# Kernel optimization log

Measured on AMD Instinct MI355X. Metric: run time of the kernel, lower is better.

## Reference

```python
import jax, jax.numpy as jnp
import numpy as np

N_GROUPS = 32
EPS = 1e-5


def group_norm(x, gamma, beta):
    b, c, h, w = x.shape
    xg = x.reshape(b, N_GROUPS, c // N_GROUPS, h, w)
    mean = xg.mean(axis=(2, 3, 4), keepdims=True)
    var = xg.var(axis=(2, 3, 4), keepdims=True)
    xn = ((xg - mean) * jax.lax.rsqrt(var + EPS)).reshape(b, c, h, w)
    return xn * gamma[None, :, None, None] + beta[None, :, None, None]


def conv1x1(x, W, b):
    # x: [b,c,h,w], W: [out,in], b: [out]
    return jnp.einsum('bchw,oc->bohw', x, W) + b[None, :, None, None]


def setup_inputs() -> dict:
    key = jax.random.key(0)
    ks = jax.random.split(key, 6)
    B, C, H, W = 8, 256, 64, 64
    s = 1.0 / np.sqrt(C)
    return {
        'x': jax.random.normal(ks[0], (B, C, H, W), dtype=jnp.float32),
        'norm_gamma': jnp.ones((C,), jnp.float32),
        'norm_beta': jnp.zeros((C,), jnp.float32),
        'Wq': jax.random.normal(ks[1], (C, C), jnp.float32) * s,
        'bq': jnp.zeros((C,), jnp.float32),
        'Wk': jax.random.normal(ks[2], (C, C), jnp.float32) * s,
        'bk': jnp.zeros((C,), jnp.float32),
        'Wv': jax.random.normal(ks[3], (C, C), jnp.float32) * s,
        'bv': jnp.zeros((C,), jnp.float32),
        'Wo': jax.random.normal(ks[4], (C, C), jnp.float32) * s,
        'bo': jnp.zeros((C,), jnp.float32),
    }


def reference(x, norm_gamma, norm_beta, Wq, bq, Wk, bk, Wv, bv, Wo, bo):
    b, c, h, w = x.shape
    hn = group_norm(x, norm_gamma, norm_beta)
    q = conv1x1(hn, Wq, bq).reshape(b, c, h * w)  # [b,c,hw]
    k = conv1x1(hn, Wk, bk).reshape(b, c, h * w)
    v = conv1x1(hn, Wv, bv).reshape(b, c, h * w)
    # scores[b,i,j] = sum_c q[b,c,i] * k[b,c,j]; scale is int(c)*-0.5
    # (faithful to the source, which multiplies by -0.5*c, NOT c**-0.5)
    scores = jnp.einsum('bci,bcj->bij', q, k) * (c * -0.5)
    attn = jax.nn.softmax(scores, axis=2)  # softmax over j (keys)
    # h_[b,c,i] = sum_j v[b,c,j] * attn[b,i,j]
    h_ = jnp.einsum('bcj,bij->bci', v, attn).reshape(b, c, h, w)
    # source applies self.out to the ORIGINAL input x and adds attention output
    return h_ + conv1x1(x, Wo, bo)
```

## Files before the change

kernel.cpp:

```cpp
#include <hip/hip_runtime.h>
#include <hip/hip_bf16.h>


typedef __attribute__((ext_vector_type(8))) short bf16x8;
typedef __attribute__((ext_vector_type(4))) short s16x4;
typedef __attribute__((ext_vector_type(8))) short s16x8;
typedef __attribute__((ext_vector_type(4))) float f32x4;

#define MFMA16(a, b, c) __builtin_amdgcn_mfma_f32_16x16x32_bf16((a), (b), (c), 0, 0, 0)

#define SCALE_Q (-184.66496523378734f)

__device__ __forceinline__ short f2bf(float f) {
  unsigned int u = __builtin_bit_cast(unsigned int, f);
  u = (u + 0x7FFFu + ((u >> 16) & 1u)) >> 16;
  return (short)(unsigned short)u;
}
__device__ __forceinline__ float bf2f(short h) {
  unsigned int u = ((unsigned int)(unsigned short)h) << 16;
  return __builtin_bit_cast(float, u);
}
__device__ __forceinline__ void async16(void* lds, const void* g) {
  __builtin_amdgcn_global_load_lds(
      (const __attribute__((address_space(1))) unsigned int*)g,
      (__attribute__((address_space(3))) unsigned int*)lds, 16, 0, 0);
}

__global__ void wsplit_k(const float* __restrict__ Wq, const float* __restrict__ Wk,
                         const float* __restrict__ Wv, const float* __restrict__ Wo,
                         short* __restrict__ whi, short* __restrict__ wlo) {
  int idx = blockIdx.x * 256 + threadIdx.x;
  int m = idx >> 16;
  int e = idx & 65535;
  const float* W = (m == 0) ? Wq : (m == 1) ? Wk : (m == 2) ? Wv : Wo;
  float v = W[e];
  short h = f2bf(v);
  whi[idx] = h;
  wlo[idx] = f2bf(v - bf2f(h));
}

__global__ void gn_stats_k(const float* __restrict__ x, float* __restrict__ stats) {
  int bg = blockIdx.x;
  int tid = threadIdx.x;
  const float* p = x + (size_t)bg * 32768;
  float s = 0.f, sq = 0.f;
  for (int it = 0; it < 32; ++it) {
    f32x4 v = *(const f32x4*)(p + (size_t)(it * 256 + tid) * 4);
    s += v[0] + v[1] + v[2] + v[3];
    sq += v[0] * v[0] + v[1] * v[1] + v[2] * v[2] + v[3] * v[3];
  }
#pragma unroll
  for (int off = 1; off < 64; off <<= 1) {
    s += __shfl_xor(s, off);
    sq += __shfl_xor(sq, off);
  }
  __shared__ float ls[4], lq[4];
  int w = tid >> 6;
  if ((tid & 63) == 0) { ls[w] = s; lq[w] = sq; }
  __syncthreads();
  if (tid == 0) {
    float S = ls[0] + ls[1] + ls[2] + ls[3];
    float Q = lq[0] + lq[1] + lq[2] + lq[3];
    float mean = S * (1.f / 32768.f);
    float var = Q * (1.f / 32768.f) - mean * mean;
    stats[bg * 2] = mean;
    stats[bg * 2 + 1] = rsqrtf(var + 1e-5f);
  }
}

__global__ void gn_apply_k(const float* __restrict__ x, const float* __restrict__ gamma,
                           const float* __restrict__ beta, const float* __restrict__ stats,
                           short* __restrict__ hn_hi, short* __restrict__ hn_lo) {
  __shared__ float tile[64 * 68];
  int tid = threadIdx.x;
  int b = blockIdx.z, c0 = blockIdx.y * 64, i0 = blockIdx.x * 64;
  int cc = tid >> 4, ich = tid & 15;
#pragma unroll
  for (int it = 0; it < 4; ++it) {
    int c = c0 + cc + it * 16;
    f32x4 vx = *(const f32x4*)(x + ((size_t)(b * 256 + c)) * 4096 + i0 + ich * 4);
    float mean = stats[(b * 32 + (c >> 3)) * 2];
    float rstd = stats[(b * 32 + (c >> 3)) * 2 + 1];
    float ga = gamma[c] * rstd;
    float be = beta[c] - mean * ga;
    f32x4 h = {vx[0] * ga + be, vx[1] * ga + be, vx[2] * ga + be, vx[3] * ga + be};
    *(f32x4*)(&tile[(cc + it * 16) * 68 + ich * 4]) = h;
  }
  __syncthreads();
  int il = tid >> 2, ch = tid & 3;
  s16x8 hv0, hv1, lv0, lv1;
#pragma unroll
  for (int u = 0; u < 16; ++u) {
    float vv = tile[(ch * 16 + u) * 68 + il];
    short h = f2bf(vv);
    short lo = f2bf(vv - bf2f(h));
    if (u < 8) { hv0[u] = h; lv0[u] = lo; } else { hv1[u - 8] = h; lv1[u - 8] = lo; }
  }
  size_t ro = ((size_t)(b * 4096 + i0 + il)) * 256 + c0 + ch * 16;
  *(s16x8*)(hn_hi + ro) = hv0;
  *(s16x8*)(hn_hi + ro + 8) = hv1;
  *(s16x8*)(hn_lo + ro) = lv0;
  *(s16x8*)(hn_lo + ro + 8) = lv1;
}

__global__ void xt_k(const float* __restrict__ x, short* __restrict__ xt) {
  __shared__ float tile[64 * 68];
  int tid = threadIdx.x;
  int b = blockIdx.z, c0 = blockIdx.y * 64, i0 = blockIdx.x * 64;
  int cc = tid >> 4, ich = tid & 15;
#pragma unroll
  for (int it = 0; it < 4; ++it) {
    int c = c0 + cc + it * 16;
    f32x4 vx = *(const f32x4*)(x + ((size_t)(b * 256 + c)) * 4096 + i0 + ich * 4);
    *(f32x4*)(&tile[(cc + it * 16) * 68 + ich * 4]) = vx;
  }
  __syncthreads();
  int il = tid >> 2, ch = tid & 3;
  s16x8 hv0, hv1;
#pragma unroll
  for (int u = 0; u < 16; ++u) {
    float vv = tile[(ch * 16 + u) * 68 + il];
    short h = f2bf(vv);
    if (u < 8) hv0[u] = h; else hv1[u - 8] = h;
  }
  size_t ro = ((size_t)(b * 4096 + i0 + il)) * 256 + c0 + ch * 16;
  *(s16x8*)(xt + ro) = hv0;
  *(s16x8*)(xt + ro + 8) = hv1;
}

__global__ __launch_bounds__(256) void proj_qk_k(
    const short* __restrict__ hn_hi, const short* __restrict__ hn_lo,
    const short* __restrict__ whi, const short* __restrict__ wlo,
    const float* __restrict__ bq, const float* __restrict__ bk,
    short* __restrict__ q_hi, short* __restrict__ q_lo,
    short* __restrict__ k_hi, short* __restrict__ k_lo) {
  int tid = threadIdx.x, w = tid >> 6, lane = tid & 63, l4 = lane & 15, g = lane >> 4;
  int iblk = blockIdx.x, y = blockIdx.y, b = blockIdx.z;
  const short* wh = whi + y * 65536;
  const short* wl = wlo + y * 65536;
  const float* bias = y ? bk : bq;
  short* ohi = (y ? k_hi : q_hi) + (size_t)b * 1048576;
  short* olo = (y ? k_lo : q_lo) + (size_t)b * 1048576;
  float scale = y ? 1.0f : SCALE_Q;
  int arow = iblk * 64 + w * 16 + l4;
  const short* ha = hn_hi + ((size_t)(b * 4096 + arow)) * 256 + g * 8;
  const short* la = hn_lo + ((size_t)(b * 4096 + arow)) * 256 + g * 8;
  f32x4 acc[16];
#pragma unroll
  for (int i = 0; i < 16; ++i) acc[i] = (f32x4){0.f, 0.f, 0.f, 0.f};
  for (int ks = 0; ks < 8; ++ks) {
    bf16x8 ah = *(const bf16x8*)(ha + ks * 32);
    bf16x8 al = *(const bf16x8*)(la + ks * 32);
#pragma unroll
    for (int ct = 0; ct < 16; ++ct) {
      bf16x8 bh = *(const bf16x8*)(wh + (ct * 16 + l4) * 256 + ks * 32 + g * 8);
      bf16x8 bl = *(const bf16x8*)(wl + (ct * 16 + l4) * 256 + ks * 32 + g * 8);
      acc[ct] = MFMA16(ah, bh, acc[ct]);
      acc[ct] = MFMA16(al, bh, acc[ct]);
      acc[ct] = MFMA16(ah, bl, acc[ct]);
    }
  }
  int orow = iblk * 64 + w * 16 + g * 4;
#pragma unroll
  for (int ct = 0; ct < 16; ++ct) {
    int c = ct * 16 + l4;
    float bsv = bias[c];
#pragma unroll
    for (int r = 0; r < 4; ++r) {
      float val = (acc[ct][r] + bsv) * scale;
      short h = f2bf(val);
      short lo = f2bf(val - bf2f(h));
      size_t off = ((size_t)(orow + r)) * 256 + c;
      ohi[off] = h;
      olo[off] = lo;
    }
  }
}

__global__ __launch_bounds__(256) void proj_v_k(
    const short* __restrict__ hn_hi, const short* __restrict__ wv_hi,
    const float* __restrict__ bv, short* __restrict__ vout) {
  int tid = threadIdx.x, w = tid >> 6, lane = tid & 63, l4 = lane & 15, g = lane >> 4;
  int jblk = blockIdx.x, cblk = blockIdx.y, b = blockIdx.z;
  int crow = cblk * 64 + w * 16 + l4;
  const short* ap = wv_hi + (size_t)crow * 256 + g * 8;
  f32x4 acc[4];
#pragma unroll
  for (int i = 0; i < 4; ++i) acc[i] = (f32x4){0.f, 0.f, 0.f, 0.f};
  for (int ks = 0; ks < 8; ++ks) {
    bf16x8 a = *(const bf16x8*)(ap + ks * 32);
#pragma unroll
    for (int jt = 0; jt < 4; ++jt) {
      bf16x8 bb = *(const bf16x8*)(hn_hi +
          ((size_t)(b * 4096 + jblk * 64 + jt * 16 + l4)) * 256 + ks * 32 + g * 8);
      acc[jt] = MFMA16(a, bb, acc[jt]);
    }
  }
#pragma unroll
  for (int jt = 0; jt < 4; ++jt) {
#pragma unroll
    for (int r = 0; r < 4; ++r) {
      int c = cblk * 64 + w * 16 + g * 4 + r;
      int j = jblk * 64 + jt * 16 + l4;
      float val = acc[jt][r] + bv[c];
      vout[((size_t)(b * 256 + c)) * 4096 + j] = f2bf(val);
    }
  }
}

__global__ __launch_bounds__(256) void outproj_k(
    const short* __restrict__ xt, const short* __restrict__ wo_hi,
    const float* __restrict__ bo, float* __restrict__ out) {
  int tid = threadIdx.x, w = tid >> 6, lane = tid & 63, l4 = lane & 15, g = lane >> 4;
  int jblk = blockIdx.x, cblk = blockIdx.y, b = blockIdx.z;
  int crow = cblk * 64 + w * 16 + l4;
  const short* ap = wo_hi + (size_t)crow * 256 + g * 8;
  f32x4 acc[4];
#pragma unroll
  for (int i = 0; i < 4; ++i) acc[i] = (f32x4){0.f, 0.f, 0.f, 0.f};
  for (int ks = 0; ks < 8; ++ks) {
    bf16x8 a = *(const bf16x8*)(ap + ks * 32);
#pragma unroll
    for (int jt = 0; jt < 4; ++jt) {
      bf16x8 bb = *(const bf16x8*)(xt +
          ((size_t)(b * 4096 + jblk * 64 + jt * 16 + l4)) * 256 + ks * 32 + g * 8);
      acc[jt] = MFMA16(a, bb, acc[jt]);
    }
  }
#pragma unroll
  for (int jt = 0; jt < 4; ++jt) {
#pragma unroll
    for (int r = 0; r < 4; ++r) {
      int c = cblk * 64 + w * 16 + g * 4 + r;
      int j = jblk * 64 + jt * 16 + l4;
      out[((size_t)(b * 256 + c)) * 4096 + j] = acc[jt][r] + bo[c];
    }
  }
}

__global__ __launch_bounds__(256, 2) void flash_k(
    const short* __restrict__ qhi, const short* __restrict__ qlo,
    const short* __restrict__ khi, const short* __restrict__ klo,
    const short* __restrict__ vv, float* __restrict__ out) {
  __shared__ short k_hi_s[8192];
  __shared__ short k_lo_s[8192];
  __shared__ short v_s[8192];
  __shared__ short p_s[2560];

  int tid = threadIdx.x, w = tid >> 6, lane = tid & 63, l4 = lane & 15, g = lane >> 4;
  int b = blockIdx.y, i0 = blockIdx.x * 64;
  size_t boff = (size_t)b * 1048576;
  const short* qh_p = qhi + boff;
  const short* ql_p = qlo + boff;
  const char* kh_g = (const char*)(khi + boff);
  const char* kl_g = (const char*)(klo + boff);
  const char* v_g = (const char*)(vv + boff);

  int qrow = i0 + w * 16 + l4;
  bf16x8 qh[8], ql[8];
#pragma unroll
  for (int ks = 0; ks < 8; ++ks) {
    qh[ks] = *(const bf16x8*)(qh_p + (size_t)qrow * 256 + ks * 32 + g * 8);
    ql[ks] = *(const bf16x8*)(ql_p + (size_t)qrow * 256 + ks * 32 + g * 8);
  }

  f32x4 oac[16];
#pragma unroll
  for (int i = 0; i < 16; ++i) oac[i] = (f32x4){0.f, 0.f, 0.f, 0.f};
  float m_cur = -1e30f, lsum = 0.f;

  int sx = (l4 & 7) << 4;
  int colx[8];
#pragma unroll
  for (int ks = 0; ks < 8; ++ks) colx[ks] = (ks * 64 + g * 16) ^ sx;
  int krow_b = l4 * 512;
  int vx = l4 * 64 + ((g ^ (l4 & 3)) << 4);
  int pwb = w * 1280 + l4 * 80 + g * 8;
  int prb = w * 1280 + l4 * 80 + g * 16;

  int ksrc[4], vsrc[4];
#pragma unroll
  for (int it = 0; it < 4; ++it) {
    int d = tid * 16 + it * 4096;
    int krow = d >> 9, kcol = d & 511;
    ksrc[it] = krow * 512 + (kcol ^ ((krow & 7) << 4));
    int vrow = d >> 6, vch = (d >> 4) & 3;
    vsrc[it] = vrow * 8192 + ((vch ^ (vrow & 3)) << 4);
  }

  char* khs = (char*)k_hi_s;
  char* kls = (char*)k_lo_s;
  char* vs = (char*)v_s;
  char* ps = (char*)p_s;

  for (int js = 0; js < 128; ++js) {
    int kgo = js * 16384;
    int vgo = js * 64;
    __syncthreads();
#pragma unroll
    for (int it = 0; it < 4; ++it) {
      int ldst = w * 1024 + it * 4096;
      async16(khs + ldst, kh_g + kgo + ksrc[it]);
      async16(kls + ldst, kl_g + kgo + ksrc[it]);
      async16(vs + ldst, v_g + vgo + vsrc[it]);
    }
    __syncthreads();

    f32x4 st0 = (f32x4){0.f, 0.f, 0.f, 0.f};
    f32x4 st1 = (f32x4){0.f, 0.f, 0.f, 0.f};
#pragma unroll
    for (int ks = 0; ks < 8; ++ks) {
      bf16x8 kh0 = *(const bf16x8*)(khs + krow_b + colx[ks]);
      bf16x8 kh1 = *(const bf16x8*)(khs + krow_b + colx[ks] + 8192);
      bf16x8 kl0 = *(const bf16x8*)(kls + krow_b + colx[ks]);
      bf16x8 kl1 = *(const bf16x8*)(kls + krow_b + colx[ks] + 8192);
      st0 = MFMA16(kh0, qh[ks], st0);
      st1 = MFMA16(kh1, qh[ks], st1);
      st0 = MFMA16(kl0, qh[ks], st0);
      st1 = MFMA16(kl1, qh[ks], st1);
      st0 = MFMA16(kh0, ql[ks], st0);
      st1 = MFMA16(kh1, ql[ks], st1);
    }

    float pmax = fmaxf(fmaxf(fmaxf(st0[0], st0[1]), fmaxf(st0[2], st0[3])),
                       fmaxf(fmaxf(st1[0], st1[1]), fmaxf(st1[2], st1[3])));
    pmax = fmaxf(pmax, __shfl_xor(pmax, 16));
    pmax = fmaxf(pmax, __shfl_xor(pmax, 32));
    if (!__all(pmax <= m_cur + 11.0f)) {
      float m_new = fmaxf(m_cur, pmax);
      float al = exp2f(m_cur - m_new);
      lsum *= al;
      int rb = g * 4;
      f32x4 av;
      av[0] = __shfl(al, rb);
      av[1] = __shfl(al, rb + 1);
      av[2] = __shfl(al, rb + 2);
      av[3] = __shfl(al, rb + 3);
#pragma unroll
      for (int ct = 0; ct < 16; ++ct) oac[ct] *= av;
      m_cur = m_new;
    }
    f32x4 e0, e1;
#pragma unroll
    for (int r = 0; r < 4; ++r) {
      e0[r] = exp2f(st0[r] - m_cur);
      e1[r] = exp2f(st1[r] - m_cur);
    }
    float lps = e0[0] + e0[1] + e0[2] + e0[3] + e1[0] + e1[1] + e1[2] + e1[3];
    lps += __shfl_xor(lps, 16);
    lps += __shfl_xor(lps, 32);
    lsum += lps;

    s16x4 pw0 = {f2bf(e0[0]), f2bf(e0[1]), f2bf(e0[2]), f2bf(e0[3])};
    s16x4 pw1 = {f2bf(e1[0]), f2bf(e1[1]), f2bf(e1[2]), f2bf(e1[3])};
    *(s16x4*)(ps + pwb) = pw0;
    *(s16x4*)(ps + pwb + 32) = pw1;
    bf16x8 pa = *(const bf16x8*)(ps + prb);
#pragma unroll
    for (int ct = 0; ct < 16; ++ct) {
      bf16x8 vb = *(const bf16x8*)(vs + vx + ct * 1024);
      oac[ct] = MFMA16(pa, vb, oac[ct]);
    }
  }

  f32x4 inv;
  {
    int rb = g * 4;
    inv[0] = 1.f / __shfl(lsum, rb);
    inv[1] = 1.f / __shfl(lsum, rb + 1);
    inv[2] = 1.f / __shfl(lsum, rb + 2);
    inv[3] = 1.f / __shfl(lsum, rb + 3);
  }
  float* ob = out + (size_t)b * 1048576;
  int irow = i0 + w * 16 + g * 4;
#pragma unroll
  for (int ct = 0; ct < 16; ++ct) {
    float* ad = ob + (size_t)(ct * 16 + l4) * 4096 + irow;
    f32x4 prev = *(const f32x4*)ad;
    f32x4 res;
#pragma unroll
    for (int r = 0; r < 4; ++r) res[r] = prev[r] + oac[ct][r] * inv[r];
    *(f32x4*)ad = res;
  }
}

extern "C" void kernel_launch(void* const* d_in, const int* in_sizes, int n_in,
                              void* d_out, int out_size, void* d_ws, size_t ws_size,
                              hipStream_t stream) {
  (void)in_sizes; (void)n_in; (void)out_size; (void)ws_size;
  const float* x = (const float*)d_in[0];
  const float* gamma = (const float*)d_in[1];
  const float* beta = (const float*)d_in[2];
  const float* Wq = (const float*)d_in[3];
  const float* bq = (const float*)d_in[4];
  const float* Wk = (const float*)d_in[5];
  const float* bk = (const float*)d_in[6];
  const float* Wv = (const float*)d_in[7];
  const float* bv = (const float*)d_in[8];
  const float* Wo = (const float*)d_in[9];
  const float* bo = (const float*)d_in[10];
  float* out = (float*)d_out;
  char* ws = (char*)d_ws;

  const size_t MB16 = 16777216;
  float* stats = (float*)(ws);
  short* whi = (short*)(ws + 4096);
  short* wlo = (short*)(ws + 4096 + 524288);
  char* base = ws + 4096 + 2 * 524288;
  short* hnhi = (short*)(base);
  short* hnlo = (short*)(base + MB16);
  short* qhi = (short*)(base + 2 * MB16);
  short* qlo = (short*)(base + 3 * MB16);
  short* khi = (short*)(base + 4 * MB16);
  short* klo = (short*)(base + 5 * MB16);
  short* vvp = (short*)(base + 6 * MB16);
  short* xt = hnhi;

  wsplit_k<<<dim3(1024), dim3(256), 0, stream>>>(Wq, Wk, Wv, Wo, whi, wlo);
  gn_stats_k<<<dim3(256), dim3(256), 0, stream>>>(x, stats);
  gn_apply_k<<<dim3(64, 4, 8), dim3(256), 0, stream>>>(x, gamma, beta, stats, hnhi, hnlo);
  proj_qk_k<<<dim3(64, 2, 8), dim3(256), 0, stream>>>(hnhi, hnlo, whi, wlo, bq, bk,
                                                      qhi, qlo, khi, klo);
  proj_v_k<<<dim3(64, 4, 8), dim3(256), 0, stream>>>(hnhi, whi + 2 * 65536, bv, vvp);
  xt_k<<<dim3(64, 4, 8), dim3(256), 0, stream>>>(x, xt);
  outproj_k<<<dim3(64, 4, 8), dim3(256), 0, stream>>>(xt, whi + 3 * 65536, bo, out);
  flash_k<<<dim3(64, 8), dim3(256), 0, stream>>>(qhi, qlo, khi, klo, vvp, out);
}
```

Before: 561.3 us.

## Fuse output projection into flash kernel and double-buffer K tiles

Removes the xt transpose and outproj kernels and computes the Wo·x projection inside the attention kernel's epilogue, adding it to the normalized attention output before a single store. The flash kernel now double-buffers K hi/lo tiles in LDS with async prefetch of the next tile, and loads V directly from global into registers. The P·V step is restructured so each wave owns a 64-channel slice for all 64 query rows, with rescale factors shared through LDS. It also raises wave priority around the score MFMAs. The exchange is an extra barrier per iteration and uncoalesced global V and x reads, which may cost more than the eliminated kernel launches and output read-modify-write.

```diff
diff --git a/kernel.cpp b/kernel.cpp
--- a/kernel.cpp
+++ b/kernel.cpp
@@ -101,31 +101,6 @@
   *(s16x8*)(hn_hi + ro + 8) = hv1;
   *(s16x8*)(hn_lo + ro) = lv0;
   *(s16x8*)(hn_lo + ro + 8) = lv1;
-}
-
-__global__ void xt_k(const float* __restrict__ x, short* __restrict__ xt) {
-  __shared__ float tile[64 * 68];
-  int tid = threadIdx.x;
-  int b = blockIdx.z, c0 = blockIdx.y * 64, i0 = blockIdx.x * 64;
-  int cc = tid >> 4, ich = tid & 15;
-#pragma unroll
-  for (int it = 0; it < 4; ++it) {
-    int c = c0 + cc + it * 16;
-    f32x4 vx = *(const f32x4*)(x + ((size_t)(b * 256 + c)) * 4096 + i0 + ich * 4);
-    *(f32x4*)(&tile[(cc + it * 16) * 68 + ich * 4]) = vx;
-  }
-  __syncthreads();
-  int il = tid >> 2, ch = tid & 3;
-  s16x8 hv0, hv1;
-#pragma unroll
-  for (int u = 0; u < 16; ++u) {
-    float vv = tile[(ch * 16 + u) * 68 + il];
-    short h = f2bf(vv);
-    if (u < 8) hv0[u] = h; else hv1[u - 8] = h;
-  }
-  size_t ro = ((size_t)(b * 4096 + i0 + il)) * 256 + c0 + ch * 16;
-  *(s16x8*)(xt + ro) = hv0;
-  *(s16x8*)(xt + ro + 8) = hv1;
 }
 
 __global__ __launch_bounds__(256) void proj_qk_k(
@@ -208,44 +183,18 @@
   }
 }
 
-__global__ __launch_bounds__(256) void outproj_k(
-    const short* __restrict__ xt, const short* __restrict__ wo_hi,
-    const float* __restrict__ bo, float* __restrict__ out) {
-  int tid = threadIdx.x, w = tid >> 6, lane = tid & 63, l4 = lane & 15, g = lane >> 4;
-  int jblk = blockIdx.x, cblk = blockIdx.y, b = blockIdx.z;
-  int crow = cblk * 64 + w * 16 + l4;
-  const short* ap = wo_hi + (size_t)crow * 256 + g * 8;
-  f32x4 acc[4];
-#pragma unroll
-  for (int i = 0; i < 4; ++i) acc[i] = (f32x4){0.f, 0.f, 0.f, 0.f};
-  for (int ks = 0; ks < 8; ++ks) {
-    bf16x8 a = *(const bf16x8*)(ap + ks * 32);
-#pragma unroll
-    for (int jt = 0; jt < 4; ++jt) {
-      bf16x8 bb = *(const bf16x8*)(xt +
-          ((size_t)(b * 4096 + jblk * 64 + jt * 16 + l4)) * 256 + ks * 32 + g * 8);
-      acc[jt] = MFMA16(a, bb, acc[jt]);
-    }
-  }
-#pragma unroll
-  for (int jt = 0; jt < 4; ++jt) {
-#pragma unroll
-    for (int r = 0; r < 4; ++r) {
-      int c = cblk * 64 + w * 16 + g * 4 + r;
-      int j = jblk * 64 + jt * 16 + l4;
-      out[((size_t)(b * 256 + c)) * 4096 + j] = acc[jt][r] + bo[c];
-    }
-  }
-}
-
-__global__ __launch_bounds__(256, 2) void flash_k(
+__global__ __launch_bounds__(256, 2) void flash3_k(
     const short* __restrict__ qhi, const short* __restrict__ qlo,
     const short* __restrict__ khi, const short* __restrict__ klo,
-    const short* __restrict__ vv, float* __restrict__ out) {
-  __shared__ short k_hi_s[8192];
-  __shared__ short k_lo_s[8192];
-  __shared__ short v_s[8192];
-  __shared__ short p_s[2560];
+    const short* __restrict__ vv, const float* __restrict__ x,
+    const short* __restrict__ wo_hi, const float* __restrict__ bo,
+    float* __restrict__ out) {
+  __shared__ short k_hi_s[2][8192];
+  __shared__ short k_lo_s[2][8192];
+  __shared__ short p_s[2048];
+  __shared__ __attribute__((aligned(16))) float albuf[64];
+  __shared__ __attribute__((aligned(16))) float flagbuf[4];
+  __shared__ __attribute__((aligned(16))) float lsmbuf[64];
 
   int tid = threadIdx.x, w = tid >> 6, lane = tid & 63, l4 = lane & 15, g = lane >> 4;
   int b = blockIdx.y, i0 = blockIdx.x * 64;
@@ -254,7 +203,7 @@
   const short* ql_p = qlo + boff;
   const char* kh_g = (const char*)(khi + boff);
   const char* kl_g = (const char*)(klo + boff);
-  const char* v_g = (const char*)(vv + boff);
+  const short* v_p = vv + boff;
 
   int qrow = i0 + w * 16 + l4;
   bf16x8 qh[8], ql[8];
@@ -264,9 +213,11 @@
     ql[ks] = *(const bf16x8*)(ql_p + (size_t)qrow * 256 + ks * 32 + g * 8);
   }
 
-  f32x4 oac[16];
-#pragma unroll
-  for (int i = 0; i < 16; ++i) oac[i] = (f32x4){0.f, 0.f, 0.f, 0.f};
+  f32x4 oac[4][4];
+#pragma unroll
+  for (int it = 0; it < 4; ++it)
+#pragma unroll
+    for (int ct = 0; ct < 4; ++ct) oac[it][ct] = (f32x4){0.f, 0.f, 0.f, 0.f};
   float m_cur = -1e30f, lsum = 0.f;
 
   int sx = (l4 & 7) << 4;
@@ -274,46 +225,55 @@
 #pragma unroll
   for (int ks = 0; ks < 8; ++ks) colx[ks] = (ks * 64 + g * 16) ^ sx;
   int krow_b = l4 * 512;
-  int vx = l4 * 64 + ((g ^ (l4 & 3)) << 4);
-  int pwb = w * 1280 + l4 * 80 + g * 8;
-  int prb = w * 1280 + l4 * 80 + g * 16;
-
-  int ksrc[4], vsrc[4];
+
+  int ksrc[4];
 #pragma unroll
   for (int it = 0; it < 4; ++it) {
     int d = tid * 16 + it * 4096;
     int krow = d >> 9, kcol = d & 511;
     ksrc[it] = krow * 512 + (kcol ^ ((krow & 7) << 4));
-    int vrow = d >> 6, vch = (d >> 4) & 3;
-    vsrc[it] = vrow * 8192 + ((vch ^ (vrow & 3)) << 4);
   }
 
   char* khs = (char*)k_hi_s;
   char* kls = (char*)k_lo_s;
-  char* vs = (char*)v_s;
   char* ps = (char*)p_s;
+  int cbase = w * 64;
+  bf16x8 vreg[4];
+
+#pragma unroll
+  for (int it = 0; it < 4; ++it) {
+    int ldst = w * 1024 + it * 4096;
+    async16(khs + ldst, kh_g + ksrc[it]);
+    async16(kls + ldst, kl_g + ksrc[it]);
+  }
 
   for (int js = 0; js < 128; ++js) {
-    int kgo = js * 16384;
-    int vgo = js * 64;
+    int cur = (js & 1) * 16384;
     __syncthreads();
-#pragma unroll
-    for (int it = 0; it < 4; ++it) {
-      int ldst = w * 1024 + it * 4096;
-      async16(khs + ldst, kh_g + kgo + ksrc[it]);
-      async16(kls + ldst, kl_g + kgo + ksrc[it]);
-      async16(vs + ldst, v_g + vgo + vsrc[it]);
-    }
-    __syncthreads();
+    if (js < 127) {
+      int kgo = (js + 1) * 16384;
+      int nxt = ((js + 1) & 1) * 16384;
+#pragma unroll
+      for (int it = 0; it < 4; ++it) {
+        int ldst = nxt + w * 1024 + it * 4096;
+        async16(khs + ldst, kh_g + kgo + ksrc[it]);
+        async16(kls + ldst, kl_g + kgo + ksrc[it]);
+      }
+    }
+#pragma unroll
+    for (int ct = 0; ct < 4; ++ct)
+      vreg[ct] = *(const bf16x8*)(v_p + (size_t)(cbase + ct * 16 + l4) * 4096 +
+                                  js * 32 + g * 8);
 
     f32x4 st0 = (f32x4){0.f, 0.f, 0.f, 0.f};
     f32x4 st1 = (f32x4){0.f, 0.f, 0.f, 0.f};
+    __builtin_amdgcn_s_setprio(1);
 #pragma unroll
     for (int ks = 0; ks < 8; ++ks) {
-      bf16x8 kh0 = *(const bf16x8*)(khs + krow_b + colx[ks]);
-      bf16x8 kh1 = *(const bf16x8*)(khs + krow_b + colx[ks] + 8192);
-      bf16x8 kl0 = *(const bf16x8*)(kls + krow_b + colx[ks]);
-      bf16x8 kl1 = *(const bf16x8*)(kls + krow_b + colx[ks] + 8192);
+      bf16x8 kh0 = *(const bf16x8*)(khs + cur + krow_b + colx[ks]);
+      bf16x8 kh1 = *(const bf16x8*)(khs + cur + krow_b + colx[ks] + 8192);
+      bf16x8 kl0 = *(const bf16x8*)(kls + cur + krow_b + colx[ks]);
+      bf16x8 kl1 = *(const bf16x8*)(kls + cur + krow_b + colx[ks] + 8192);
       st0 = MFMA16(kh0, qh[ks], st0);
       st1 = MFMA16(kh1, qh[ks], st1);
       st0 = MFMA16(kl0, qh[ks], st0);
@@ -321,23 +281,18 @@
       st0 = MFMA16(kh0, ql[ks], st0);
       st1 = MFMA16(kh1, ql[ks], st1);
     }
+    __builtin_amdgcn_s_setprio(0);
 
     float pmax = fmaxf(fmaxf(fmaxf(st0[0], st0[1]), fmaxf(st0[2], st0[3])),
                        fmaxf(fmaxf(st1[0], st1[1]), fmaxf(st1[2], st1[3])));
     pmax = fmaxf(pmax, __shfl_xor(pmax, 16));
     pmax = fmaxf(pmax, __shfl_xor(pmax, 32));
-    if (!__all(pmax <= m_cur + 11.0f)) {
+    float alpha = 1.0f;
+    bool upd = !__all(pmax <= m_cur + 11.0f);
+    if (upd) {
       float m_new = fmaxf(m_cur, pmax);
-      float al = exp2f(m_cur - m_new);
-      lsum *= al;
-      int rb = g * 4;
-      f32x4 av;
-      av[0] = __shfl(al, rb);
-      av[1] = __shfl(al, rb + 1);
-      av[2] = __shfl(al, rb + 2);
-      av[3] = __shfl(al, rb + 3);
-#pragma unroll
-      for (int ct = 0; ct < 16; ++ct) oac[ct] *= av;
+      alpha = exp2f(m_cur - m_new);
+      lsum *= alpha;
       m_cur = m_new;
     }
     f32x4 e0, e1;
@@ -353,34 +308,75 @@
 
     s16x4 pw0 = {f2bf(e0[0]), f2bf(e0[1]), f2bf(e0[2]), f2bf(e0[3])};
     s16x4 pw1 = {f2bf(e1[0]), f2bf(e1[1]), f2bf(e1[2]), f2bf(e1[3])};
-    *(s16x4*)(ps + pwb) = pw0;
-    *(s16x4*)(ps + pwb + 32) = pw1;
-    bf16x8 pa = *(const bf16x8*)(ps + prb);
-#pragma unroll
-    for (int ct = 0; ct < 16; ++ct) {
-      bf16x8 vb = *(const bf16x8*)(vs + vx + ct * 1024);
-      oac[ct] = MFMA16(pa, vb, oac[ct]);
-    }
-  }
-
-  f32x4 inv;
-  {
-    int rb = g * 4;
-    inv[0] = 1.f / __shfl(lsum, rb);
-    inv[1] = 1.f / __shfl(lsum, rb + 1);
-    inv[2] = 1.f / __shfl(lsum, rb + 2);
-    inv[3] = 1.f / __shfl(lsum, rb + 3);
+    int wb = (w * 16 + l4) * 64 + g * 8;
+    *(s16x4*)(ps + wb) = pw0;
+    *(s16x4*)(ps + wb + 32) = pw1;
+    if (lane < 16) albuf[w * 16 + lane] = alpha;
+    if (lane == 0) flagbuf[w] = upd ? 1.f : 0.f;
+
+    __syncthreads();
+
+    f32x4 fl = *(const f32x4*)(&flagbuf[0]);
+    if (fl[0] + fl[1] + fl[2] + fl[3] > 0.f) {
+#pragma unroll
+      for (int it = 0; it < 4; ++it) {
+        f32x4 av = *(const f32x4*)(&albuf[it * 16 + g * 4]);
+#pragma unroll
+        for (int ct = 0; ct < 4; ++ct)
+#pragma unroll
+          for (int r = 0; r < 4; ++r) oac[it][ct][r] *= av[r];
+      }
+    }
+#pragma unroll
+    for (int it = 0; it < 4; ++it) {
+      bf16x8 pf = *(const bf16x8*)(ps + (it * 16 + l4) * 64 + g * 16);
+#pragma unroll
+      for (int ct = 0; ct < 4; ++ct) oac[it][ct] = MFMA16(pf, vreg[ct], oac[it][ct]);
+    }
+  }
+
+  if (lane < 16) lsmbuf[w * 16 + lane] = lsum;
+  __syncthreads();
+#pragma unroll
+  for (int it = 0; it < 4; ++it) {
+    f32x4 lv = *(const f32x4*)(&lsmbuf[it * 16 + g * 4]);
+    f32x4 iv = {1.f / lv[0], 1.f / lv[1], 1.f / lv[2], 1.f / lv[3]};
+#pragma unroll
+    for (int ct = 0; ct < 4; ++ct)
+#pragma unroll
+      for (int r = 0; r < 4; ++r) oac[it][ct][r] *= iv[r];
+  }
+  const float* xb = x + (size_t)b * 1048576;
+  for (int ks = 0; ks < 8; ++ks) {
+    bf16x8 af[4], bfr[4];
+#pragma unroll
+    for (int it = 0; it < 4; ++it) {
+#pragma unroll
+      for (int e = 0; e < 8; ++e) {
+        float xv = xb[(size_t)(ks * 32 + g * 8 + e) * 4096 + i0 + it * 16 + l4];
+        af[it][e] = f2bf(xv);
+      }
+    }
+#pragma unroll
+    for (int ct = 0; ct < 4; ++ct)
+      bfr[ct] = *(const bf16x8*)(wo_hi + (cbase + ct * 16 + l4) * 256 + ks * 32 + g * 8);
+#pragma unroll
+    for (int it = 0; it < 4; ++it)
+#pragma unroll
+      for (int ct = 0; ct < 4; ++ct) oac[it][ct] = MFMA16(af[it], bfr[ct], oac[it][ct]);
   }
   float* ob = out + (size_t)b * 1048576;
-  int irow = i0 + w * 16 + g * 4;
-#pragma unroll
-  for (int ct = 0; ct < 16; ++ct) {
-    float* ad = ob + (size_t)(ct * 16 + l4) * 4096 + irow;
-    f32x4 prev = *(const f32x4*)ad;
-    f32x4 res;
-#pragma unroll
-    for (int r = 0; r < 4; ++r) res[r] = prev[r] + oac[ct][r] * inv[r];
-    *(f32x4*)ad = res;
+#pragma unroll
+  for (int ct = 0; ct < 4; ++ct) {
+    float bov = bo[cbase + ct * 16 + l4];
+#pragma unroll
+    for (int it = 0; it < 4; ++it) {
+      float* ad = ob + (size_t)(cbase + ct * 16 + l4) * 4096 + i0 + it * 16 + g * 4;
+      f32x4 res;
+#pragma unroll
+      for (int r = 0; r < 4; ++r) res[r] = oac[it][ct][r] + bov;
+      *(f32x4*)ad = res;
+    }
   }
 }
 
@@ -414,7 +410,6 @@
   short* khi = (short*)(base + 4 * MB16);
   short* klo = (short*)(base + 5 * MB16);
   short* vvp = (short*)(base + 6 * MB16);
-  short* xt = hnhi;
 
   wsplit_k<<<dim3(1024), dim3(256), 0, stream>>>(Wq, Wk, Wv, Wo, whi, wlo);
   gn_stats_k<<<dim3(256), dim3(256), 0, stream>>>(x, stats);
@@ -422,7 +417,6 @@
   proj_qk_k<<<dim3(64, 2, 8), dim3(256), 0, stream>>>(hnhi, hnlo, whi, wlo, bq, bk,
                                                       qhi, qlo, khi, klo);
   proj_v_k<<<dim3(64, 4, 8), dim3(256), 0, stream>>>(hnhi, whi + 2 * 65536, bv, vvp);
-  xt_k<<<dim3(64, 4, 8), dim3(256), 0, stream>>>(x, xt);
-  outproj_k<<<dim3(64, 4, 8), dim3(256), 0, stream>>>(xt, whi + 3 * 65536, bo, out);
-  flash_k<<<dim3(64, 8), dim3(256), 0, stream>>>(qhi, qlo, khi, klo, vvp, out);
-}
+  flash3_k<<<dim3(64, 8), dim3(256), 0, stream>>>(qhi, qlo, khi, klo, vvp, x,
+                                                  whi + 3 * 65536, bo, out);
+}
```

After: 537.3 us. -4.3%, faster.
